# Kernel tuning notes

Hardware: AMD Instinct MI355X
Metric: run time of the kernel (lower is better)

The kernel has to match this reference:

```python
import jax, jax.numpy as jnp
from jax import lax
import numpy as np

LEVELS = 3
HU_RANGE = 240.0 - (-160.0)          # hu_window = (-160, 240)
BASE_THR = 40.0 / HU_RANGE           # threshold / hu_range
MAD_TO_SIGMA = 1.0 / 0.6745


def haar2(x):
    """Single-level 2D orthonormal Haar DWT. x: [B, h, w] (h, w even).
    Returns cA, cH, cV, cD each [B, h//2, w//2]. Sign conventions are
    irrelevant to this loss (only |coeff| matters in MAD and L1 terms)."""
    B, h, w = x.shape
    x = x.reshape(B, h // 2, 2, w // 2, 2)
    a = x[:, :, 0, :, 0]
    b = x[:, :, 0, :, 1]
    c = x[:, :, 1, :, 0]
    d = x[:, :, 1, :, 1]
    cA = (a + b + c + d) * 0.5
    cH = (a + b - c - d) * 0.5
    cV = (a - b + c - d) * 0.5
    cD = (a - b - c + d) * 0.5
    return cA, cH, cV, cD


def soft_threshold(c, t):
    return jnp.sign(c) * jnp.maximum(jnp.abs(c) - t, 0.0)


def setup_inputs() -> dict:
    key = jax.random.key(0)
    pred = jax.random.normal(key, (128, 1, 512, 512), dtype=jnp.float32)
    return {"pred": pred}


def reference(pred):
    x = pred[:, 0]                     # [B, H, W]
    B = x.shape[0]

    # Multi-level decomposition: details[0] = finest, details[-1] = coarsest.
    details = []
    cA = x
    for _ in range(LEVELS):
        cA, cH, cV, cD = haar2(cA)
        details.append((cH, cV, cD))

    # pywt coeffs[1] is the COARSEST detail triple -> MAD noise estimate.
    cH, cV, cD = details[-1]
    all_details = jnp.concatenate(
        [cH.reshape(B, -1), cV.reshape(B, -1), cD.reshape(B, -1)], axis=1)
    sigma = jnp.median(jnp.abs(all_details), axis=1) * MAD_TO_SIGMA  # [B]
    adaptive_thr = jnp.clip(sigma * 2.5, BASE_THR * 0.5, BASE_THR * 2.0)
    adaptive_thr = lax.stop_gradient(adaptive_thr)                   # [B]

    # level_idx = 1 corresponds to pywt coeffs[1] (coarsest) = details[-1].
    total = jnp.zeros((B,), dtype=x.dtype)
    for level_idx in range(1, LEVELS + 1):
        cH, cV, cD = details[LEVELS - level_idx]
        t = (adaptive_thr / (2.0 ** (level_idx - 1)))[:, None, None]
        lvl = jnp.zeros((B,), dtype=x.dtype)
        for c in (cH, cV, cD):
            target = lax.stop_gradient(soft_threshold(c, t))
            lvl = lvl + jnp.mean(jnp.abs(c - target), axis=(1, 2))
        total = total + (1.0 / level_idx) * lvl / 3.0

    loss = jnp.mean(total)             # sum over batch / valid_samples (all valid)
    avg_noise = jnp.mean(sigma)
    return loss, avg_noise
```

## Files before the change

kernel.cpp:

```cpp
#include <hip/hip_runtime.h>
#include <stdint.h>


static constexpr int BATCH = 128;
static constexpr int W = 512;
static constexpr int N3 = 64 * 64;
static constexpr int NDET = 3 * N3;

__device__ __forceinline__ float block_reduce_sum(float v, float* lds) {
    #pragma unroll
    for (int off = 32; off > 0; off >>= 1)
        v += __shfl_down(v, off, 64);
    const int lane = threadIdx.x & 63;
    const int wave = threadIdx.x >> 6;
    if (lane == 0) lds[wave] = v;
    __syncthreads();
    if (threadIdx.x == 0) {
        float s = 0.0f;
        const int nw = blockDim.x >> 6;
        for (int w = 0; w < nw; ++w) s += lds[w];
        lds[0] = s;
    }
    __syncthreads();
    return lds[0];
}

__device__ __forceinline__ float wavelet_block_loss(
        const float* __restrict__ blk, float t1, float t2, float t3,
        float* detH, float* detV, float* detD, bool write_det) {
    float cA1[4][4];
    float s1 = 0.0f, s2 = 0.0f, s3 = 0.0f;

    #pragma unroll
    for (int rr = 0; rr < 4; ++rr) {
        const float4 r0a = *(const float4*)(blk + (size_t)(2 * rr) * W);
        const float4 r0b = *(const float4*)(blk + (size_t)(2 * rr) * W + 4);
        const float4 r1a = *(const float4*)(blk + (size_t)(2 * rr + 1) * W);
        const float4 r1b = *(const float4*)(blk + (size_t)(2 * rr + 1) * W + 4);
        const float top[8] = {r0a.x, r0a.y, r0a.z, r0a.w, r0b.x, r0b.y, r0b.z, r0b.w};
        const float bot[8] = {r1a.x, r1a.y, r1a.z, r1a.w, r1b.x, r1b.y, r1b.z, r1b.w};
        #pragma unroll
        for (int cc = 0; cc < 4; ++cc) {
            const float a = top[2 * cc], b = top[2 * cc + 1];
            const float c = bot[2 * cc], d = bot[2 * cc + 1];
            const float sab = a + b, scd = c + d, dab = a - b, dcd = c - d;
            const float cA = 0.5f * (sab + scd);
            const float cH = 0.5f * (sab - scd);
            const float cV = 0.5f * (dab + dcd);
            const float cD = 0.5f * (dab - dcd);
            s1 += fminf(fabsf(cH), t1) + fminf(fabsf(cV), t1) + fminf(fabsf(cD), t1);
            cA1[rr][cc] = cA;
        }
    }

    float cA2[2][2];
    #pragma unroll
    for (int rr = 0; rr < 2; ++rr) {
        #pragma unroll
        for (int cc = 0; cc < 2; ++cc) {
            const float a = cA1[2 * rr][2 * cc],     b = cA1[2 * rr][2 * cc + 1];
            const float c = cA1[2 * rr + 1][2 * cc], d = cA1[2 * rr + 1][2 * cc + 1];
            const float sab = a + b, scd = c + d, dab = a - b, dcd = c - d;
            const float cA = 0.5f * (sab + scd);
            const float cH = 0.5f * (sab - scd);
            const float cV = 0.5f * (dab + dcd);
            const float cD = 0.5f * (dab - dcd);
            s2 += fminf(fabsf(cH), t2) + fminf(fabsf(cV), t2) + fminf(fabsf(cD), t2);
            cA2[rr][cc] = cA;
        }
    }

    {
        const float a = cA2[0][0], b = cA2[0][1], c = cA2[1][0], d = cA2[1][1];
        const float sab = a + b, scd = c + d, dab = a - b, dcd = c - d;
        const float cH = 0.5f * (sab - scd);
        const float cV = 0.5f * (dab + dcd);
        const float cD = 0.5f * (dab - dcd);
        const float aH = fabsf(cH), aV = fabsf(cV), aD = fabsf(cD);
        s3 = fminf(aH, t3) + fminf(aV, t3) + fminf(aD, t3);
        if (write_det) { *detH = aH; *detV = aV; *detD = aD; }
    }

    const float w1 = 1.0f / (9.0f * 65536.0f);
    const float w2 = 1.0f / (6.0f * 16384.0f);
    const float w3 = 1.0f / (3.0f * 4096.0f);
    return s1 * w1 + s2 * w2 + s3 * w3;
}

__global__ __launch_bounds__(256) void pass_a(const float* __restrict__ x,
                                              float* __restrict__ spec_loss,
                                              float* __restrict__ det3) {
    const int b = blockIdx.y;
    const int p = blockIdx.x * 256 + threadIdx.x;
    const int i3 = p >> 6, j3 = p & 63;
    const float* blk = x + (size_t)b * W * W + (size_t)(i3 * 8) * W + j3 * 8;

    const float BASE = 40.0f / 400.0f;
    const float t3 = BASE * 2.0f, t2 = t3 * 0.5f, t1 = t3 * 0.25f;

    float* det = det3 + (size_t)b * NDET;
    const float part = wavelet_block_loss(blk, t1, t2, t3,
                                          &det[0 * N3 + p], &det[1 * N3 + p],
                                          &det[2 * N3 + p], true);
    __shared__ float lds[8];
    const float tot = block_reduce_sum(part, lds);
    if (threadIdx.x == 0) atomicAdd(&spec_loss[b], tot);
}

__global__ __launch_bounds__(256) void pass_b(const float* __restrict__ det3,
                                              float* __restrict__ sigma_out,
                                              float* __restrict__ t_out) {
    const int b = blockIdx.x;
    const float* det = det3 + (size_t)b * NDET;

    uint32_t vals[48];
    #pragma unroll
    for (int i = 0; i < 48; ++i)
        vals[i] = __float_as_uint(det[threadIdx.x + 256 * i]);

    __shared__ uint32_t red[8];
    uint32_t lo1 = 0, hi1 = 0x7F800000u;
    uint32_t lo2 = 0, hi2 = 0x7F800000u;
    while (lo1 < hi1 || lo2 < hi2) {
        const uint32_t mid1 = (lo1 + hi1) >> 1;
        const uint32_t mid2 = (lo2 + hi2) >> 1;
        uint32_t c1 = 0, c2 = 0;
        #pragma unroll
        for (int i = 0; i < 48; ++i) {
            c1 += (vals[i] <= mid1);
            c2 += (vals[i] <= mid2);
        }
        uint32_t packed = c1 | (c2 << 16);
        #pragma unroll
        for (int off = 32; off > 0; off >>= 1)
            packed += __shfl_down(packed, off, 64);
        const int lane = threadIdx.x & 63, wave = threadIdx.x >> 6;
        if (lane == 0) red[wave] = packed;
        __syncthreads();
        if (threadIdx.x == 0) red[0] = red[0] + red[1] + red[2] + red[3];
        __syncthreads();
        packed = red[0];
        __syncthreads();
        c1 = packed & 0xFFFFu;
        c2 = packed >> 16;
        if (lo1 < hi1) { if (c1 >= 6144u) hi1 = mid1; else lo1 = mid1 + 1; }
        if (lo2 < hi2) { if (c2 >= 6145u) hi2 = mid2; else lo2 = mid2 + 1; }
    }

    if (threadIdx.x == 0) {
        const float v1 = __uint_as_float(lo1);
        const float v2 = __uint_as_float(lo2);
        const float med = 0.5f * (v1 + v2);
        const float M2S = (float)(1.0 / 0.6745);
        const float sig = med * M2S;
        sigma_out[b] = sig;
        const float BASE = 40.0f / 400.0f;
        t_out[b] = fminf(fmaxf(sig * 2.5f, BASE * 0.5f), BASE * 2.0f);
    }
}

__global__ __launch_bounds__(256) void pass_c(const float* __restrict__ x,
                                              const float* __restrict__ t_in,
                                              float* __restrict__ fix_loss) {
    const int b = blockIdx.y;
    const float BASE = 40.0f / 400.0f;
    const float t = t_in[b];
    if (t == BASE * 2.0f) return;

    const int p = blockIdx.x * 256 + threadIdx.x;
    const int i3 = p >> 6, j3 = p & 63;
    const float* blk = x + (size_t)b * W * W + (size_t)(i3 * 8) * W + j3 * 8;

    const float part = wavelet_block_loss(blk, t * 0.25f, t * 0.5f, t,
                                          nullptr, nullptr, nullptr, false);
    __shared__ float lds[8];
    const float tot = block_reduce_sum(part, lds);
    if (threadIdx.x == 0) atomicAdd(&fix_loss[b], tot);
}

__global__ __launch_bounds__(128) void finalize(const float* __restrict__ spec,
                                                const float* __restrict__ fix,
                                                const float* __restrict__ sigma,
                                                const float* __restrict__ t_in,
                                                float* __restrict__ out) {
    __shared__ float lds[8];
    const float BASE = 40.0f / 400.0f;
    const int i = threadIdx.x;
    const float lb = (t_in[i] == BASE * 2.0f) ? spec[i] : fix[i];
    const float sg = sigma[i];
    const float ls = block_reduce_sum(lb, lds);
    __syncthreads();
    const float ss = block_reduce_sum(sg, lds);
    if (threadIdx.x == 0) {
        out[0] = ls * (1.0f / 128.0f);
        out[1] = ss * (1.0f / 128.0f);
    }
}

extern "C" void kernel_launch(void* const* d_in, const int* in_sizes, int n_in,
                              void* d_out, int out_size, void* d_ws, size_t ws_size,
                              hipStream_t stream) {
    const float* x = (const float*)d_in[0];
    float* ws = (float*)d_ws;
    float* spec  = ws;
    float* fix   = ws + 128;
    float* sigma = ws + 256;
    float* t     = ws + 384;
    float* det3  = ws + 512;

    hipMemsetAsync(spec, 0, 256 * sizeof(float), stream);

    dim3 grid(16, BATCH);
    pass_a<<<grid, 256, 0, stream>>>(x, spec, det3);
    pass_b<<<BATCH, 256, 0, stream>>>(det3, sigma, t);
    pass_c<<<grid, 256, 0, stream>>>(x, t, fix);
    finalize<<<1, 128, 0, stream>>>(spec, fix, sigma, t, (float*)d_out);
}
```

Measured before the change: 229.5 us.

## Fuse wavelet passes into one kernel with last-block-done atomic counters

Merges the spectral-loss pass, the per-batch median search, the conditional recompute and the final reduction into a single kernel. Each batch's last finishing block, detected via an atomic counter, computes the median and threshold, then recomputes the loss only if needed. A global last block then produces the final outputs. This removes kernel launch gaps and lets median searches overlap with other batches' main work, at the cost of threadfence/atomic overhead and serialized recompute within a single block when the threshold is not clamped.

```diff
diff --git a/kernel.cpp b/kernel.cpp
--- a/kernel.cpp
+++ b/kernel.cpp
@@ -17,12 +17,13 @@
     __syncthreads();
     if (threadIdx.x == 0) {
         float s = 0.0f;
-        const int nw = blockDim.x >> 6;
-        for (int w = 0; w < nw; ++w) s += lds[w];
+        for (int w = 0; w < 4; ++w) s += lds[w];
         lds[0] = s;
     }
     __syncthreads();
-    return lds[0];
+    const float r = lds[0];
+    __syncthreads();
+    return r;
 }
 
 __device__ __forceinline__ float wavelet_block_loss(
@@ -87,38 +88,50 @@
     return s1 * w1 + s2 * w2 + s3 * w3;
 }
 
-__global__ __launch_bounds__(256) void pass_a(const float* __restrict__ x,
-                                              float* __restrict__ spec_loss,
-                                              float* __restrict__ det3) {
-    const int b = blockIdx.y;
-    const int p = blockIdx.x * 256 + threadIdx.x;
-    const int i3 = p >> 6, j3 = p & 63;
-    const float* blk = x + (size_t)b * W * W + (size_t)(i3 * 8) * W + j3 * 8;
+__global__ __launch_bounds__(256) void wavelet_fused(
+        const float* __restrict__ x, uint32_t* __restrict__ cnt,
+        float* __restrict__ partials, float* __restrict__ loss_final,
+        float* __restrict__ sigma_final, float* __restrict__ det3,
+        float* __restrict__ out) {
+    __shared__ float lds[8];
+    __shared__ uint32_t red[8];
+    __shared__ int flag;
+
+    const int sub = blockIdx.x;
+    const int b   = blockIdx.y;
+    const int tid = threadIdx.x;
 
     const float BASE = 40.0f / 400.0f;
-    const float t3 = BASE * 2.0f, t2 = t3 * 0.5f, t1 = t3 * 0.25f;
-
-    float* det = det3 + (size_t)b * NDET;
-    const float part = wavelet_block_loss(blk, t1, t2, t3,
-                                          &det[0 * N3 + p], &det[1 * N3 + p],
-                                          &det[2 * N3 + p], true);
-    __shared__ float lds[8];
-    const float tot = block_reduce_sum(part, lds);
-    if (threadIdx.x == 0) atomicAdd(&spec_loss[b], tot);
-}
-
-__global__ __launch_bounds__(256) void pass_b(const float* __restrict__ det3,
-                                              float* __restrict__ sigma_out,
-                                              float* __restrict__ t_out) {
-    const int b = blockIdx.x;
+    const float TTOP = BASE * 2.0f;
+
+    {
+        const int p = sub * 256 + tid;
+        const int i3 = p >> 6, j3 = p & 63;
+        const float* blk = x + (size_t)b * W * W + (size_t)(i3 * 8) * W + j3 * 8;
+        float* det = det3 + (size_t)b * NDET;
+        const float part = wavelet_block_loss(blk, TTOP * 0.25f, TTOP * 0.5f, TTOP,
+                                              &det[0 * N3 + p], &det[1 * N3 + p],
+                                              &det[2 * N3 + p], true);
+        const float tot = block_reduce_sum(part, lds);
+        if (tid == 0) partials[b * 16 + sub] = tot;
+    }
+
+    __threadfence();
+    __syncthreads();
+    if (tid == 0) {
+        const uint32_t old = atomicAdd(&cnt[b], 1u);
+        flag = (old == 15u);
+    }
+    __syncthreads();
+    if (!flag) return;
+    __threadfence();
+
     const float* det = det3 + (size_t)b * NDET;
-
     uint32_t vals[48];
     #pragma unroll
     for (int i = 0; i < 48; ++i)
-        vals[i] = __float_as_uint(det[threadIdx.x + 256 * i]);
-
-    __shared__ uint32_t red[8];
+        vals[i] = __float_as_uint(det[tid + 256 * i]);
+
     uint32_t lo1 = 0, hi1 = 0x7F800000u;
     uint32_t lo2 = 0, hi2 = 0x7F800000u;
     while (lo1 < hi1 || lo2 < hi2) {
@@ -134,10 +147,10 @@
         #pragma unroll
         for (int off = 32; off > 0; off >>= 1)
             packed += __shfl_down(packed, off, 64);
-        const int lane = threadIdx.x & 63, wave = threadIdx.x >> 6;
+        const int lane = tid & 63, wave = tid >> 6;
         if (lane == 0) red[wave] = packed;
         __syncthreads();
-        if (threadIdx.x == 0) red[0] = red[0] + red[1] + red[2] + red[3];
+        if (tid == 0) red[0] = red[0] + red[1] + red[2] + red[3];
         __syncthreads();
         packed = red[0];
         __syncthreads();
@@ -146,54 +159,48 @@
         if (lo1 < hi1) { if (c1 >= 6144u) hi1 = mid1; else lo1 = mid1 + 1; }
         if (lo2 < hi2) { if (c2 >= 6145u) hi2 = mid2; else lo2 = mid2 + 1; }
     }
-
-    if (threadIdx.x == 0) {
-        const float v1 = __uint_as_float(lo1);
-        const float v2 = __uint_as_float(lo2);
-        const float med = 0.5f * (v1 + v2);
-        const float M2S = (float)(1.0 / 0.6745);
-        const float sig = med * M2S;
-        sigma_out[b] = sig;
-        const float BASE = 40.0f / 400.0f;
-        t_out[b] = fminf(fmaxf(sig * 2.5f, BASE * 0.5f), BASE * 2.0f);
-    }
-}
-
-__global__ __launch_bounds__(256) void pass_c(const float* __restrict__ x,
-                                              const float* __restrict__ t_in,
-                                              float* __restrict__ fix_loss) {
-    const int b = blockIdx.y;
-    const float BASE = 40.0f / 400.0f;
-    const float t = t_in[b];
-    if (t == BASE * 2.0f) return;
-
-    const int p = blockIdx.x * 256 + threadIdx.x;
-    const int i3 = p >> 6, j3 = p & 63;
-    const float* blk = x + (size_t)b * W * W + (size_t)(i3 * 8) * W + j3 * 8;
-
-    const float part = wavelet_block_loss(blk, t * 0.25f, t * 0.5f, t,
-                                          nullptr, nullptr, nullptr, false);
-    __shared__ float lds[8];
-    const float tot = block_reduce_sum(part, lds);
-    if (threadIdx.x == 0) atomicAdd(&fix_loss[b], tot);
-}
-
-__global__ __launch_bounds__(128) void finalize(const float* __restrict__ spec,
-                                                const float* __restrict__ fix,
-                                                const float* __restrict__ sigma,
-                                                const float* __restrict__ t_in,
-                                                float* __restrict__ out) {
-    __shared__ float lds[8];
-    const float BASE = 40.0f / 400.0f;
-    const int i = threadIdx.x;
-    const float lb = (t_in[i] == BASE * 2.0f) ? spec[i] : fix[i];
-    const float sg = sigma[i];
+    const float med = 0.5f * (__uint_as_float(lo1) + __uint_as_float(lo2));
+    const float sig = med * (float)(1.0 / 0.6745);
+    const float t = fminf(fmaxf(sig * 2.5f, BASE * 0.5f), TTOP);
+
+    float loss_b;
+    if (t == TTOP) {
+        float v = (tid < 16) ? partials[b * 16 + tid] : 0.0f;
+        loss_b = block_reduce_sum(v, lds);
+    } else {
+        float part = 0.0f;
+        #pragma unroll 1
+        for (int k = 0; k < 16; ++k) {
+            const int p = k * 256 + tid;
+            const int i3 = p >> 6, j3 = p & 63;
+            const float* blk = x + (size_t)b * W * W + (size_t)(i3 * 8) * W + j3 * 8;
+            part += wavelet_block_loss(blk, t * 0.25f, t * 0.5f, t,
+                                       nullptr, nullptr, nullptr, false);
+        }
+        loss_b = block_reduce_sum(part, lds);
+    }
+
+    if (tid == 0) {
+        loss_final[b] = loss_b;
+        sigma_final[b] = sig;
+    }
+    __threadfence();
+    __syncthreads();
+    if (tid == 0) {
+        const uint32_t old = atomicAdd(&cnt[BATCH], 1u);
+        flag = (old == (uint32_t)(BATCH - 1));
+    }
+    __syncthreads();
+    if (!flag) return;
+    __threadfence();
+
+    float lb = (tid < BATCH) ? loss_final[tid] : 0.0f;
+    float sg = (tid < BATCH) ? sigma_final[tid] : 0.0f;
     const float ls = block_reduce_sum(lb, lds);
-    __syncthreads();
     const float ss = block_reduce_sum(sg, lds);
-    if (threadIdx.x == 0) {
-        out[0] = ls * (1.0f / 128.0f);
-        out[1] = ss * (1.0f / 128.0f);
+    if (tid == 0) {
+        out[0] = ls * (1.0f / (float)BATCH);
+        out[1] = ss * (1.0f / (float)BATCH);
     }
 }
 
@@ -202,17 +209,15 @@
                               hipStream_t stream) {
     const float* x = (const float*)d_in[0];
     float* ws = (float*)d_ws;
-    float* spec  = ws;
-    float* fix   = ws + 128;
-    float* sigma = ws + 256;
-    float* t     = ws + 384;
-    float* det3  = ws + 512;
-
-    hipMemsetAsync(spec, 0, 256 * sizeof(float), stream);
+    uint32_t* cnt     = (uint32_t*)ws;
+    float* partials   = ws + 160;
+    float* loss_final = ws + 2304;
+    float* sigma_final= ws + 2432;
+    float* det3       = ws + 2560;
+
+    hipMemsetAsync(cnt, 0, 129 * sizeof(uint32_t), stream);
 
     dim3 grid(16, BATCH);
-    pass_a<<<grid, 256, 0, stream>>>(x, spec, det3);
-    pass_b<<<BATCH, 256, 0, stream>>>(det3, sigma, t);
-    pass_c<<<grid, 256, 0, stream>>>(x, t, fix);
-    finalize<<<1, 128, 0, stream>>>(spec, fix, sigma, t, (float*)d_out);
-}
+    wavelet_fused<<<grid, 256, 0, stream>>>(x, cnt, partials, loss_final,
+                                            sigma_final, det3, (float*)d_out);
+}
```

New measurement: 667.1 us. +190.7%, slower.
